# Optimization experiments

Hardware: AMD Instinct MI355X
Metric: run time of the kernel (lower is better)

## Reference

```python
import jax, jax.numpy as jnp
import numpy as np

N = 50000      # nodes
E = 800000     # edges (before self-loops)
F_IN = 128     # input node features
H = 4          # attention heads
C = 32         # hidden channels per head (concat width = H*C = 128)
CLS = 40       # num classes (layer 4, concat=False -> mean over heads)
NEG_SLOPE = 0.2


def setup_inputs() -> dict:
    key = jax.random.key(0)
    ks = jax.random.split(key, 16)
    w = lambda k, shape: (jax.random.normal(k, shape, jnp.float32) * 0.1)
    return {
        "x": jax.random.normal(ks[0], (N, F_IN), jnp.float32),
        "edge_index": jax.random.randint(ks[1], (2, E), 0, N),
        "W1": w(ks[2], (F_IN, H * C)), "att_src1": w(ks[3], (H, C)), "att_dst1": w(ks[4], (H, C)), "b1": jnp.zeros((H * C,), jnp.float32),
        "W2": w(ks[5], (H * C, H * C)), "att_src2": w(ks[6], (H, C)), "att_dst2": w(ks[7], (H, C)), "b2": jnp.zeros((H * C,), jnp.float32),
        "W3": w(ks[8], (H * C, H * C)), "att_src3": w(ks[9], (H, C)), "att_dst3": w(ks[10], (H, C)), "b3": jnp.zeros((H * C,), jnp.float32),
        "W4": w(ks[11], (H * C, H * CLS)), "att_src4": w(ks[12], (H, CLS)), "att_dst4": w(ks[13], (H, CLS)), "b4": jnp.zeros((CLS,), jnp.float32),
    }


def _gat(x, W, a_src, a_dst, b, src, dst, n, heads, ch, concat):
    # Linear transform, per-head view: [n, heads, ch]
    h = (x @ W).reshape(n, heads, ch)
    # per-node scalar attention terms [n, heads]
    es = (h * a_src).sum(-1)
    ed = (h * a_dst).sum(-1)
    # edge logits: alpha_j (source) + alpha_i (target), leaky relu (PyG GATConv)
    e = jax.nn.leaky_relu(es[src] + ed[dst], NEG_SLOPE)  # [Etot, heads]
    # segment softmax over incoming edges of each dst node (self-loops guarantee >=1 edge)
    m = jax.ops.segment_max(e, dst, num_segments=n)
    ealpha = jnp.exp(e - m[dst])
    denom = jax.ops.segment_sum(ealpha, dst, num_segments=n)
    alpha = ealpha / denom[dst]
    # weighted message aggregation (scatter-add)
    out = jax.ops.segment_sum(h[src] * alpha[:, :, None], dst, num_segments=n)
    out = out.reshape(n, heads * ch) if concat else out.mean(axis=1)
    return out + b


def reference(x, edge_index, W1, att_src1, att_dst1, b1, W2, att_src2, att_dst2, b2,
              W3, att_src3, att_dst3, b3, W4, att_src4, att_dst4, b4):
    n = x.shape[0]
    loop = jnp.arange(n)
    src = jnp.concatenate([edge_index[0], loop])  # add self-loops (PyG default)
    dst = jnp.concatenate([edge_index[1], loop])
    # dropout layers are identity in eval mode (training=False)
    h = _gat(x, W1, att_src1, att_dst1, b1, src, dst, n, H, C, True)
    h = jax.nn.relu(h)
    h = _gat(h, W2, att_src2, att_dst2, b2, src, dst, n, H, C, True)
    h = jax.nn.relu(h)
    h = _gat(h, W3, att_src3, att_dst3, b3, src, dst, n, H, C, True)
    h = jax.nn.relu(h)
    h = _gat(h, W4, att_src4, att_dst4, b4, src, dst, n, H, CLS, False)
    return h
```

## Files before the change

### kernel.cpp

```cpp
#include <hip/hip_runtime.h>
#include <math.h>

#define NN 50000
#define EE 800000
#define ET (EE + NN)
#define NCHK ((NN + 255) / 256)
#define NEG 0.2f

__device__ __forceinline__ float lrelu(float x) { return x > 0.f ? x : NEG * x; }

typedef __bf16 bf16x8 __attribute__((ext_vector_type(8)));
typedef float f32x4 __attribute__((ext_vector_type(4)));


__global__ __launch_bounds__(256) void k_hist(const int* __restrict__ eidx, int* __restrict__ cnt) {
    int i = blockIdx.x * 256 + threadIdx.x;
    if (i < EE) atomicAdd(&cnt[eidx[EE + i]], 1);
}

__global__ __launch_bounds__(256) void k_csum(const int* __restrict__ cnt, int* __restrict__ csums) {
    __shared__ int sh[256];
    int t = threadIdx.x, i = blockIdx.x * 256 + t;
    sh[t] = (i < NN) ? cnt[i] + 1 : 0;
    __syncthreads();
    for (int off = 128; off > 0; off >>= 1) {
        if (t < off) sh[t] += sh[t + off];
        __syncthreads();
    }
    if (t == 0) csums[blockIdx.x] = sh[0];
}

__global__ __launch_bounds__(256) void k_cscan(int* __restrict__ csums, int* __restrict__ rowptr) {
    __shared__ int sh[256];
    int t = threadIdx.x;
    sh[t] = (t < NCHK) ? csums[t] : 0;
    __syncthreads();
    for (int off = 1; off < 256; off <<= 1) {
        int x = (t >= off) ? sh[t - off] : 0;
        __syncthreads();
        sh[t] += x;
        __syncthreads();
    }
    int ex = (t == 0) ? 0 : sh[t - 1];
    if (t < NCHK) csums[t] = ex;
    if (t == 0) rowptr[NN] = ET;
}

__global__ __launch_bounds__(256) void k_chscan(const int* __restrict__ cnt, const int* __restrict__ csums,
                                                int* __restrict__ rowptr, int* __restrict__ cursor) {
    __shared__ int sh[256];
    int t = threadIdx.x, b = blockIdx.x, i = b * 256 + t;
    int v = (i < NN) ? cnt[i] + 1 : 0;
    sh[t] = v;
    __syncthreads();
    for (int off = 1; off < 256; off <<= 1) {
        int x = (t >= off) ? sh[t - off] : 0;
        __syncthreads();
        sh[t] += x;
        __syncthreads();
    }
    int ex = (t == 0 ? 0 : sh[t - 1]) + csums[b];
    if (i < NN) { rowptr[i] = ex; cursor[i] = ex; }
}

__global__ __launch_bounds__(256) void k_scatter(const int* __restrict__ eidx,
                                                 int* __restrict__ cursor, int* __restrict__ ssrc) {
    int i = blockIdx.x * 256 + threadIdx.x;
    if (i >= ET) return;
    int s, d;
    if (i < EE) { s = eidx[i]; d = eidx[EE + i]; } else { s = d = i - EE; }
    int pos = atomicAdd(&cursor[d], 1);
    ssrc[pos] = s;
}


template <int NOUT>
__global__ __launch_bounds__(256) void k_wsplit(const float* __restrict__ Wm,
                                                __bf16* __restrict__ Whi, __bf16* __restrict__ Wlo) {
    int i = blockIdx.x * 256 + threadIdx.x;
    if (i >= 128 * NOUT) return;
    int k = i / NOUT, c = i - k * NOUT;
    float v = Wm[i];
    __bf16 hi = (__bf16)v;
    __bf16 lo = (__bf16)(v - (float)hi);
    size_t off = ((size_t)(k >> 3) * NOUT + c) * 8 + (k & 7);
    Whi[off] = hi;
    Wlo[off] = lo;
}


template <int NOUT, bool FUSE>
__global__ __launch_bounds__(256) void k_gemm2(const float* __restrict__ X,
                                               const __bf16* __restrict__ Whi,
                                               const __bf16* __restrict__ Wlo,
                                               float* __restrict__ Y,
                                               const float* __restrict__ asrc,
                                               const float* __restrict__ adst,
                                               float* __restrict__ es, float* __restrict__ ed) {
    constexpr int NT = NOUT / 16;
    int tid = threadIdx.x;
    int w = tid >> 6, l = tid & 63;
    int col = l & 15, kg = l >> 4;
    int rb = blockIdx.x * 64;
    int arow = rb + w * 16 + col;
    int rclamp = arow < NN ? arow : NN - 1;
    f32x4 acc[NT];
    #pragma unroll
    for (int t = 0; t < NT; ++t) acc[t] = (f32x4){0.f, 0.f, 0.f, 0.f};

    #pragma unroll
    for (int c4 = 0; c4 < 4; ++c4) {
        float4 aA = *reinterpret_cast<const float4*>(&X[(size_t)rclamp * 128 + c4 * 32 + kg * 8]);
        float4 aB = *reinterpret_cast<const float4*>(&X[(size_t)rclamp * 128 + c4 * 32 + kg * 8 + 4]);
        float av[8] = {aA.x, aA.y, aA.z, aA.w, aB.x, aB.y, aB.z, aB.w};
        bf16x8 ahi, alo;
        #pragma unroll
        for (int j = 0; j < 8; ++j) {
            __bf16 h = (__bf16)av[j];
            ahi[j] = h;
            alo[j] = (__bf16)(av[j] - (float)h);
        }
        const __bf16* bh = Whi + ((size_t)(c4 * 4 + kg) * NOUT) * 8;
        const __bf16* bl = Wlo + ((size_t)(c4 * 4 + kg) * NOUT) * 8;
        #pragma unroll
        for (int t = 0; t < NT; ++t) {
            bf16x8 bhi = *reinterpret_cast<const bf16x8*>(bh + (t * 16 + col) * 8);
            bf16x8 blo = *reinterpret_cast<const bf16x8*>(bl + (t * 16 + col) * 8);
            acc[t] = __builtin_amdgcn_mfma_f32_16x16x32_bf16(ahi, bhi, acc[t], 0, 0, 0);
            acc[t] = __builtin_amdgcn_mfma_f32_16x16x32_bf16(alo, bhi, acc[t], 0, 0, 0);
            acc[t] = __builtin_amdgcn_mfma_f32_16x16x32_bf16(ahi, blo, acc[t], 0, 0, 0);
        }
    }

    #pragma unroll
    for (int t = 0; t < NT; ++t) {
        int cc = t * 16 + col;
        #pragma unroll
        for (int i = 0; i < 4; ++i) {
            int rr = rb + w * 16 + kg * 4 + i;
            if (rr < NN) Y[(size_t)rr * NOUT + cc] = acc[t][i];
        }
    }

    if constexpr (FUSE) {
        float pes[4][4], ped[4][4];
        #pragma unroll
        for (int h = 0; h < 4; ++h)
            #pragma unroll
            for (int i = 0; i < 4; ++i) { pes[h][i] = 0.f; ped[h][i] = 0.f; }
        #pragma unroll
        for (int t = 0; t < 8; ++t) {
            float as = asrc[t * 16 + col];
            float ad = adst[t * 16 + col];
            int h = t >> 1;
            #pragma unroll
            for (int i = 0; i < 4; ++i) {
                pes[h][i] += acc[t][i] * as;
                ped[h][i] += acc[t][i] * ad;
            }
        }
        #pragma unroll
        for (int off = 1; off < 16; off <<= 1) {
            #pragma unroll
            for (int h = 0; h < 4; ++h)
                #pragma unroll
                for (int i = 0; i < 4; ++i) {
                    pes[h][i] += __shfl_xor(pes[h][i], off);
                    ped[h][i] += __shfl_xor(ped[h][i], off);
                }
        }
        if (col == 0) {
            #pragma unroll
            for (int i = 0; i < 4; ++i) {
                int rr = rb + w * 16 + kg * 4 + i;
                if (rr < NN) {
                    #pragma unroll
                    for (int h = 0; h < 4; ++h) {
                        es[rr * 4 + h] = pes[h][i];
                        ed[rr * 4 + h] = ped[h][i];
                    }
                }
            }
        }
    }
}


template <int CH>
__global__ __launch_bounds__(256) void k_attn_scal(const float* __restrict__ Hf,
                                                   const float* __restrict__ asrc,
                                                   const float* __restrict__ adst,
                                                   float* __restrict__ es, float* __restrict__ ed) {
    int i = blockIdx.x * 256 + threadIdx.x;
    if (i >= NN * 4) return;
    int h = i & 3, n = i >> 2;
    const float4* row = reinterpret_cast<const float4*>(Hf + (size_t)n * (4 * CH) + h * CH);
    const float4* As  = reinterpret_cast<const float4*>(asrc + h * CH);
    const float4* Ad  = reinterpret_cast<const float4*>(adst + h * CH);
    float s = 0.f, d = 0.f;
    #pragma unroll
    for (int c = 0; c < CH / 4; ++c) {
        float4 v = row[c], a = As[c], b = Ad[c];
        s += v.x * a.x + v.y * a.y + v.z * a.z + v.w * a.w;
        d += v.x * b.x + v.y * b.y + v.z * b.z + v.w * b.w;
    }
    es[i] = s;
    ed[i] = d;
}


__global__ __launch_bounds__(256) void k_agg128(const float* __restrict__ Hf,
                                                const float* __restrict__ es, const float* __restrict__ ed,
                                                const int* __restrict__ rowptr, const int* __restrict__ ssrc,
                                                const float* __restrict__ bias, float* __restrict__ Yout) {
    int wid = (blockIdx.x * 256 + threadIdx.x) >> 6;
    int lane = threadIdx.x & 63;
    if (wid >= NN) return;
    int n = wid;
    int beg = rowptr[n], end = rowptr[n + 1];
    int h1 = lane & 3;
    int eoff = lane >> 2;
    float edv = ed[n * 4 + h1];

    float m = -1e30f, dsum = 0.f;
    for (int idx = beg + eoff; idx < end; idx += 16) {
        int s = ssrc[idx];
        float e = lrelu(es[s * 4 + h1] + edv);
        float M = fmaxf(m, e);
        dsum = dsum * __expf(m - M) + __expf(e - M);
        m = M;
    }
    #pragma unroll
    for (int off = 4; off < 64; off <<= 1) {
        float om = __shfl_xor(m, off);
        float od = __shfl_xor(dsum, off);
        float M = fmaxf(m, om);
        dsum = dsum * __expf(m - M) + od * __expf(om - M);
        m = M;
    }
    float invd = 1.f / dsum;

    int q = lane & 7;
    int eg8 = lane >> 3;
    f32x4 acc4[4];
    #pragma unroll
    for (int i = 0; i < 4; ++i) acc4[i] = (f32x4){0.f, 0.f, 0.f, 0.f};

    int nch = (end - beg + 15) >> 4;
    int base = beg;
    for (int ch = 0; ch < nch; ++ch, base += 16) {
        int myIdx = base + eoff;
        int s = ssrc[myIdx < end ? myIdx : end - 1];
        float e = lrelu(es[s * 4 + h1] + edv);
        float alpha = (myIdx < end) ? __expf(e - m) * invd : 0.f;
        #pragma unroll
        for (int hb = 0; hb < 2; ++hb) {
            int e16 = hb * 8 + eg8;
            int se = __shfl(s, e16 * 4);
            const float* rowp = Hf + (size_t)se * 128 + q * 4;
            #pragma unroll
            for (int i = 0; i < 4; ++i) {
                float p = __shfl(alpha, e16 * 4 + i);
                float4 v = *reinterpret_cast<const float4*>(rowp + i * 32);
                acc4[i].x += p * v.x;
                acc4[i].y += p * v.y;
                acc4[i].z += p * v.z;
                acc4[i].w += p * v.w;
            }
        }
    }

    #pragma unroll
    for (int off = 8; off < 64; off <<= 1) {
        #pragma unroll
        for (int i = 0; i < 4; ++i) {
            acc4[i].x += __shfl_xor(acc4[i].x, off);
            acc4[i].y += __shfl_xor(acc4[i].y, off);
            acc4[i].z += __shfl_xor(acc4[i].z, off);
            acc4[i].w += __shfl_xor(acc4[i].w, off);
        }
    }
    if (lane < 8) {
        #pragma unroll
        for (int i = 0; i < 4; ++i) {
            int c0 = 32 * i + 4 * lane;
            float4 bv = *reinterpret_cast<const float4*>(&bias[c0]);
            float4 o;
            o.x = fmaxf(acc4[i].x + bv.x, 0.f);
            o.y = fmaxf(acc4[i].y + bv.y, 0.f);
            o.z = fmaxf(acc4[i].z + bv.z, 0.f);
            o.w = fmaxf(acc4[i].w + bv.w, 0.f);
            *reinterpret_cast<float4*>(&Yout[(size_t)n * 128 + c0]) = o;
        }
    }
}


__global__ __launch_bounds__(256) void k_agg160_mean(const float* __restrict__ Hf,
                                                     const float* __restrict__ es, const float* __restrict__ ed,
                                                     const int* __restrict__ rowptr, const int* __restrict__ ssrc,
                                                     const float* __restrict__ b4, float* __restrict__ out) {
    __shared__ float buf[4][160];
    int wid = (blockIdx.x * 256 + threadIdx.x) >> 6;
    int lane = threadIdx.x & 63;
    int w = threadIdx.x >> 6;
    if (wid >= NN) return;
    int n = wid;
    int beg = rowptr[n], end = rowptr[n + 1];
    int h1 = lane & 3;
    int eoff = lane >> 2;
    float edv = ed[n * 4 + h1];

    float m = -1e30f, dsum = 0.f;
    for (int idx = beg + eoff; idx < end; idx += 16) {
        int s = ssrc[idx];
        float e = lrelu(es[s * 4 + h1] + edv);
        float M = fmaxf(m, e);
        dsum = dsum * __expf(m - M) + __expf(e - M);
        m = M;
    }
    #pragma unroll
    for (int off = 4; off < 64; off <<= 1) {
        float om = __shfl_xor(m, off);
        float od = __shfl_xor(dsum, off);
        float M = fmaxf(m, om);
        dsum = dsum * __expf(m - M) + od * __expf(om - M);
        m = M;
    }
    float invd = 1.f / dsum;

    int q = lane & 7;
    int eg8 = lane >> 3;
    int hh[5];
    #pragma unroll
    for (int i = 0; i < 5; ++i) hh[i] = (i * 8 + q) / 10;
    f32x4 acc4[5];
    #pragma unroll
    for (int i = 0; i < 5; ++i) acc4[i] = (f32x4){0.f, 0.f, 0.f, 0.f};

    int nch = (end - beg + 15) >> 4;
    int base = beg;
    for (int ch = 0; ch < nch; ++ch, base += 16) {
        int myIdx = base + eoff;
        int s = ssrc[myIdx < end ? myIdx : end - 1];
        float e = lrelu(es[s * 4 + h1] + edv);
        float alpha = (myIdx < end) ? __expf(e - m) * invd : 0.f;
        #pragma unroll
        for (int hb = 0; hb < 2; ++hb) {
            int e16 = hb * 8 + eg8;
            int se = __shfl(s, e16 * 4);
            const float* rowp = Hf + (size_t)se * 160 + q * 4;
            #pragma unroll
            for (int i = 0; i < 5; ++i) {
                float p = __shfl(alpha, e16 * 4 + hh[i]);
                float4 v = *reinterpret_cast<const float4*>(rowp + i * 32);
                acc4[i].x += p * v.x;
                acc4[i].y += p * v.y;
                acc4[i].z += p * v.z;
                acc4[i].w += p * v.w;
            }
        }
    }

    #pragma unroll
    for (int off = 8; off < 64; off <<= 1) {
        #pragma unroll
        for (int i = 0; i < 5; ++i) {
            acc4[i].x += __shfl_xor(acc4[i].x, off);
            acc4[i].y += __shfl_xor(acc4[i].y, off);
            acc4[i].z += __shfl_xor(acc4[i].z, off);
            acc4[i].w += __shfl_xor(acc4[i].w, off);
        }
    }
    if (lane < 8) {
        #pragma unroll
        for (int i = 0; i < 5; ++i)
            *reinterpret_cast<float4*>(&buf[w][32 * i + 4 * lane]) = (float4){acc4[i].x, acc4[i].y, acc4[i].z, acc4[i].w};
    }
    __builtin_amdgcn_wave_barrier();
    if (lane < 40) {
        float v = 0.25f * (buf[w][lane] + buf[w][lane + 40] + buf[w][lane + 80] + buf[w][lane + 120]) + b4[lane];
        out[(size_t)n * 40 + lane] = v;
    }
}


extern "C" void kernel_launch(void* const* d_in, const int* in_sizes, int n_in,
                              void* d_out, int out_size, void* d_ws, size_t ws_size,
                              hipStream_t stream) {
    const float* x    = (const float*)d_in[0];
    const int*   eidx = (const int*)d_in[1];
    const float* W[4]    = {(const float*)d_in[2], (const float*)d_in[6], (const float*)d_in[10], (const float*)d_in[14]};
    const float* asrc[4] = {(const float*)d_in[3], (const float*)d_in[7], (const float*)d_in[11], (const float*)d_in[15]};
    const float* adst[4] = {(const float*)d_in[4], (const float*)d_in[8], (const float*)d_in[12], (const float*)d_in[16]};
    const float* bias[4] = {(const float*)d_in[5], (const float*)d_in[9], (const float*)d_in[13], (const float*)d_in[17]};
    float* out = (float*)d_out;

    float* hA = (float*)d_ws;
    float* hB = hA + (size_t)NN * 160;
    float* es = hB + (size_t)NN * 160;
    float* ed = es + (size_t)NN * 4;
    int* rowptr = (int*)(ed + (size_t)NN * 4);
    int* cnt    = rowptr + (NN + 1);
    int* cursor = cnt + NN;
    int* ssrc   = cursor + NN;
    int* csums  = ssrc + ET;
    __bf16* wsp = (__bf16*)(csums + 256);
    __bf16* Whi[4], *Wlo[4];
    {
        __bf16* p = wsp;
        for (int i = 0; i < 4; ++i) {
            int sz = 128 * (i == 3 ? 160 : 128);
            Whi[i] = p; p += sz;
            Wlo[i] = p; p += sz;
        }
    }

    hipMemsetAsync(cnt, 0, NN * sizeof(int), stream);
    k_hist<<<(EE + 255) / 256, 256, 0, stream>>>(eidx, cnt);
    k_csum<<<NCHK, 256, 0, stream>>>(cnt, csums);
    k_cscan<<<1, 256, 0, stream>>>(csums, rowptr);
    k_chscan<<<NCHK, 256, 0, stream>>>(cnt, csums, rowptr, cursor);
    k_scatter<<<(ET + 255) / 256, 256, 0, stream>>>(eidx, cursor, ssrc);

    k_wsplit<128><<<(128 * 128 + 255) / 256, 256, 0, stream>>>(W[0], Whi[0], Wlo[0]);
    k_wsplit<128><<<(128 * 128 + 255) / 256, 256, 0, stream>>>(W[1], Whi[1], Wlo[1]);
    k_wsplit<128><<<(128 * 128 + 255) / 256, 256, 0, stream>>>(W[2], Whi[2], Wlo[2]);
    k_wsplit<160><<<(128 * 160 + 255) / 256, 256, 0, stream>>>(W[3], Whi[3], Wlo[3]);

    int gemmBlocks = (NN + 63) / 64;
    int aggBlocks = (NN * 64 + 255) / 256;

    k_gemm2<128, true><<<gemmBlocks, 256, 0, stream>>>(x, Whi[0], Wlo[0], hA, asrc[0], adst[0], es, ed);
    k_agg128<<<aggBlocks, 256, 0, stream>>>(hA, es, ed, rowptr, ssrc, bias[0], hB);

    k_gemm2<128, true><<<gemmBlocks, 256, 0, stream>>>(hB, Whi[1], Wlo[1], hA, asrc[1], adst[1], es, ed);
    k_agg128<<<aggBlocks, 256, 0, stream>>>(hA, es, ed, rowptr, ssrc, bias[1], hB);

    k_gemm2<128, true><<<gemmBlocks, 256, 0, stream>>>(hB, Whi[2], Wlo[2], hA, asrc[2], adst[2], es, ed);
    k_agg128<<<aggBlocks, 256, 0, stream>>>(hA, es, ed, rowptr, ssrc, bias[2], hB);

    k_gemm2<160, false><<<gemmBlocks, 256, 0, stream>>>(hB, Whi[3], Wlo[3], hA, nullptr, nullptr, nullptr, nullptr);
    k_attn_scal<40><<<(NN * 4 + 255) / 256, 256, 0, stream>>>(hA, asrc[3], adst[3], es, ed);
    k_agg160_mean<<<aggBlocks, 256, 0, stream>>>(hA, es, ed, rowptr, ssrc, bias[3], out);
}
```

Measured before the change: 500.9 us.

## Merge scan and weight-split launches, widen GEMM tiles, fuse layer-4 attention scalars

Result: faster. 473.8 us (-5.4%).

```diff
diff --git a/kernel.cpp b/kernel.cpp
--- a/kernel.cpp
+++ b/kernel.cpp
@@ -30,37 +30,27 @@
     if (t == 0) csums[blockIdx.x] = sh[0];
 }
 
-__global__ __launch_bounds__(256) void k_cscan(int* __restrict__ csums, int* __restrict__ rowptr) {
-    __shared__ int sh[256];
-    int t = threadIdx.x;
-    sh[t] = (t < NCHK) ? csums[t] : 0;
-    __syncthreads();
-    for (int off = 1; off < 256; off <<= 1) {
-        int x = (t >= off) ? sh[t - off] : 0;
-        __syncthreads();
-        sh[t] += x;
-        __syncthreads();
-    }
-    int ex = (t == 0) ? 0 : sh[t - 1];
-    if (t < NCHK) csums[t] = ex;
-    if (t == 0) rowptr[NN] = ET;
-}
-
 __global__ __launch_bounds__(256) void k_chscan(const int* __restrict__ cnt, const int* __restrict__ csums,
                                                 int* __restrict__ rowptr, int* __restrict__ cursor) {
     __shared__ int sh[256];
+    __shared__ int shc[256];
     int t = threadIdx.x, b = blockIdx.x, i = b * 256 + t;
     int v = (i < NN) ? cnt[i] + 1 : 0;
     sh[t] = v;
+    shc[t] = (t < NCHK) ? csums[t] : 0;
     __syncthreads();
     for (int off = 1; off < 256; off <<= 1) {
-        int x = (t >= off) ? sh[t - off] : 0;
+        int x1 = (t >= off) ? sh[t - off] : 0;
+        int x2 = (t >= off) ? shc[t - off] : 0;
         __syncthreads();
-        sh[t] += x;
+        sh[t] += x1;
+        shc[t] += x2;
         __syncthreads();
     }
-    int ex = (t == 0 ? 0 : sh[t - 1]) + csums[b];
+    int cbase = (b == 0) ? 0 : shc[b - 1];
+    int ex = (t == 0 ? 0 : sh[t - 1]) + cbase;
     if (i < NN) { rowptr[i] = ex; cursor[i] = ex; }
+    if (b == 0 && t == 0) rowptr[NN] = ET;
 }
 
 __global__ __launch_bounds__(256) void k_scatter(const int* __restrict__ eidx,
@@ -74,23 +64,28 @@
 }
 
 
-template <int NOUT>
-__global__ __launch_bounds__(256) void k_wsplit(const float* __restrict__ Wm,
-                                                __bf16* __restrict__ Whi, __bf16* __restrict__ Wlo) {
+__global__ __launch_bounds__(256) void k_wsplit_all(const float* __restrict__ W0, const float* __restrict__ W1,
+                                                    const float* __restrict__ W2, const float* __restrict__ W3,
+                                                    __bf16* __restrict__ wsp) {
     int i = blockIdx.x * 256 + threadIdx.x;
-    if (i >= 128 * NOUT) return;
-    int k = i / NOUT, c = i - k * NOUT;
-    float v = Wm[i];
+    const float* Wm; int NOUT, j; size_t base, sz;
+    if (i < 16384)      { Wm = W0; NOUT = 128; j = i;          base = 0;     sz = 16384; }
+    else if (i < 32768) { Wm = W1; NOUT = 128; j = i - 16384;  base = 32768; sz = 16384; }
+    else if (i < 49152) { Wm = W2; NOUT = 128; j = i - 32768;  base = 65536; sz = 16384; }
+    else if (i < 69632) { Wm = W3; NOUT = 160; j = i - 49152;  base = 98304; sz = 20480; }
+    else return;
+    float v = Wm[j];
+    int k = j / NOUT, c = j - k * NOUT;
     __bf16 hi = (__bf16)v;
     __bf16 lo = (__bf16)(v - (float)hi);
-    size_t off = ((size_t)(k >> 3) * NOUT + c) * 8 + (k & 7);
-    Whi[off] = hi;
-    Wlo[off] = lo;
+    size_t off = base + ((size_t)(k >> 3) * NOUT + c) * 8 + (k & 7);
+    wsp[off] = hi;
+    wsp[off + sz] = lo;
 }
 
 
 template <int NOUT, bool FUSE>
-__global__ __launch_bounds__(256) void k_gemm2(const float* __restrict__ X,
+__global__ __launch_bounds__(256) void k_gemm3(const float* __restrict__ X,
                                                const __bf16* __restrict__ Whi,
                                                const __bf16* __restrict__ Wlo,
                                                float* __restrict__ Y,
@@ -98,27 +93,35 @@
                                                const float* __restrict__ adst,
                                                float* __restrict__ es, float* __restrict__ ed) {
     constexpr int NT = NOUT / 16;
+    constexpr int CH = NOUT / 4;
     int tid = threadIdx.x;
     int w = tid >> 6, l = tid & 63;
     int col = l & 15, kg = l >> 4;
-    int rb = blockIdx.x * 64;
-    int arow = rb + w * 16 + col;
-    int rclamp = arow < NN ? arow : NN - 1;
-    f32x4 acc[NT];
-    #pragma unroll
-    for (int t = 0; t < NT; ++t) acc[t] = (f32x4){0.f, 0.f, 0.f, 0.f};
+    int rb = blockIdx.x * 128 + w * 32;
+    int r0 = rb + col, r1 = rb + 16 + col;
+    int rc0 = r0 < NN ? r0 : NN - 1;
+    int rc1 = r1 < NN ? r1 : NN - 1;
+
+    f32x4 acc0[NT], acc1[NT];
+    #pragma unroll
+    for (int t = 0; t < NT; ++t) { acc0[t] = (f32x4){0,0,0,0}; acc1[t] = (f32x4){0,0,0,0}; }
 
     #pragma unroll
     for (int c4 = 0; c4 < 4; ++c4) {
-        float4 aA = *reinterpret_cast<const float4*>(&X[(size_t)rclamp * 128 + c4 * 32 + kg * 8]);
-        float4 aB = *reinterpret_cast<const float4*>(&X[(size_t)rclamp * 128 + c4 * 32 + kg * 8 + 4]);
-        float av[8] = {aA.x, aA.y, aA.z, aA.w, aB.x, aB.y, aB.z, aB.w};
-        bf16x8 ahi, alo;
-        #pragma unroll
-        for (int j = 0; j < 8; ++j) {
-            __bf16 h = (__bf16)av[j];
-            ahi[j] = h;
-            alo[j] = (__bf16)(av[j] - (float)h);
+        bf16x8 ah0, al0, ah1, al1;
+        {
+            float4 aA = *reinterpret_cast<const float4*>(&X[(size_t)rc0 * 128 + c4 * 32 + kg * 8]);
+            float4 aB = *reinterpret_cast<const float4*>(&X[(size_t)rc0 * 128 + c4 * 32 + kg * 8 + 4]);
+            float av[8] = {aA.x, aA.y, aA.z, aA.w, aB.x, aB.y, aB.z, aB.w};
+            #pragma unroll
+            for (int j = 0; j < 8; ++j) { __bf16 h = (__bf16)av[j]; ah0[j] = h; al0[j] = (__bf16)(av[j] - (float)h); }
+        }
+        {
+            float4 aA = *reinterpret_cast<const float4*>(&X[(size_t)rc1 * 128 + c4 * 32 + kg * 8]);
+            float4 aB = *reinterpret_cast<const float4*>(&X[(size_t)rc1 * 128 + c4 * 32 + kg * 8 + 4]);
+            float av[8] = {aA.x, aA.y, aA.z, aA.w, aB.x, aB.y, aB.z, aB.w};
+            #pragma unroll
+            for (int j = 0; j < 8; ++j) { __bf16 h = (__bf16)av[j]; ah1[j] = h; al1[j] = (__bf16)(av[j] - (float)h); }
         }
         const __bf16* bh = Whi + ((size_t)(c4 * 4 + kg) * NOUT) * 8;
         const __bf16* bl = Wlo + ((size_t)(c4 * 4 + kg) * NOUT) * 8;
@@ -126,9 +129,12 @@
         for (int t = 0; t < NT; ++t) {
             bf16x8 bhi = *reinterpret_cast<const bf16x8*>(bh + (t * 16 + col) * 8);
             bf16x8 blo = *reinterpret_cast<const bf16x8*>(bl + (t * 16 + col) * 8);
-            acc[t] = __builtin_amdgcn_mfma_f32_16x16x32_bf16(ahi, bhi, acc[t], 0, 0, 0);
-            acc[t] = __builtin_amdgcn_mfma_f32_16x16x32_bf16(alo, bhi, acc[t], 0, 0, 0);
-            acc[t] = __builtin_amdgcn_mfma_f32_16x16x32_bf16(ahi, blo, acc[t], 0, 0, 0);
+            acc0[t] = __builtin_amdgcn_mfma_f32_16x16x32_bf16(ah0, bhi, acc0[t], 0, 0, 0);
+            acc0[t] = __builtin_amdgcn_mfma_f32_16x16x32_bf16(al0, bhi, acc0[t], 0, 0, 0);
+            acc0[t] = __builtin_amdgcn_mfma_f32_16x16x32_bf16(ah0, blo, acc0[t], 0, 0, 0);
+            acc1[t] = __builtin_amdgcn_mfma_f32_16x16x32_bf16(ah1, bhi, acc1[t], 0, 0, 0);
+            acc1[t] = __builtin_amdgcn_mfma_f32_16x16x32_bf16(al1, bhi, acc1[t], 0, 0, 0);
+            acc1[t] = __builtin_amdgcn_mfma_f32_16x16x32_bf16(ah1, blo, acc1[t], 0, 0, 0);
         }
     }
 
@@ -137,75 +143,74 @@
         int cc = t * 16 + col;
         #pragma unroll
         for (int i = 0; i < 4; ++i) {
-            int rr = rb + w * 16 + kg * 4 + i;
-            if (rr < NN) Y[(size_t)rr * NOUT + cc] = acc[t][i];
+            int ra = rb + kg * 4 + i;
+            int rbq = rb + 16 + kg * 4 + i;
+            if (ra < NN)  Y[(size_t)ra  * NOUT + cc] = acc0[t][i];
+            if (rbq < NN) Y[(size_t)rbq * NOUT + cc] = acc1[t][i];
         }
     }
 
     if constexpr (FUSE) {
-        float pes[4][4], ped[4][4];
-        #pragma unroll
-        for (int h = 0; h < 4; ++h)
-            #pragma unroll
-            for (int i = 0; i < 4; ++i) { pes[h][i] = 0.f; ped[h][i] = 0.f; }
-        #pragma unroll
-        for (int t = 0; t < 8; ++t) {
+        float pes[2][4][4], ped[2][4][4];
+        #pragma unroll
+        for (int rt = 0; rt < 2; ++rt)
+            #pragma unroll
+            for (int h = 0; h < 4; ++h)
+                #pragma unroll
+                for (int i = 0; i < 4; ++i) { pes[rt][h][i] = 0.f; ped[rt][h][i] = 0.f; }
+        #pragma unroll
+        for (int t = 0; t < NT; ++t) {
             float as = asrc[t * 16 + col];
             float ad = adst[t * 16 + col];
-            int h = t >> 1;
-            #pragma unroll
-            for (int i = 0; i < 4; ++i) {
-                pes[h][i] += acc[t][i] * as;
-                ped[h][i] += acc[t][i] * ad;
-            }
-        }
-        #pragma unroll
-        for (int off = 1; off < 16; off <<= 1) {
-            #pragma unroll
-            for (int h = 0; h < 4; ++h)
+            int hA = (t * 16) / CH;
+            int hB = (t * 16 + 15) / CH;
+            if (hA == hB) {
                 #pragma unroll
                 for (int i = 0; i < 4; ++i) {
-                    pes[h][i] += __shfl_xor(pes[h][i], off);
-                    ped[h][i] += __shfl_xor(ped[h][i], off);
+                    pes[0][hA][i] += acc0[t][i] * as;  ped[0][hA][i] += acc0[t][i] * ad;
+                    pes[1][hA][i] += acc1[t][i] * as;  ped[1][hA][i] += acc1[t][i] * ad;
                 }
+            } else {
+                bool isB = (col >= (hB * CH - t * 16));
+                #pragma unroll
+                for (int i = 0; i < 4; ++i) {
+                    float vs0 = acc0[t][i] * as, vd0 = acc0[t][i] * ad;
+                    float vs1 = acc1[t][i] * as, vd1 = acc1[t][i] * ad;
+                    pes[0][hA][i] += isB ? 0.f : vs0;  pes[0][hB][i] += isB ? vs0 : 0.f;
+                    ped[0][hA][i] += isB ? 0.f : vd0;  ped[0][hB][i] += isB ? vd0 : 0.f;
+                    pes[1][hA][i] += isB ? 0.f : vs1;  pes[1][hB][i] += isB ? vs1 : 0.f;
+                    ped[1][hA][i] += isB ? 0.f : vd1;  ped[1][hB][i] += isB ? vd1 : 0.f;
+                }
+            }
+        }
+        #pragma unroll
+        for (int off = 1; off < 16; off <<= 1) {
+            #pragma unroll
+            for (int rt = 0; rt < 2; ++rt)
+                #pragma unroll
+                for (int h = 0; h < 4; ++h)
+                    #pragma unroll
+                    for (int i = 0; i < 4; ++i) {
+                        pes[rt][h][i] += __shfl_xor(pes[rt][h][i], off);
+                        ped[rt][h][i] += __shfl_xor(ped[rt][h][i], off);
+                    }
         }
         if (col == 0) {
             #pragma unroll
-            for (int i = 0; i < 4; ++i) {
-                int rr = rb + w * 16 + kg * 4 + i;
-                if (rr < NN) {
-                    #pragma unroll
-                    for (int h = 0; h < 4; ++h) {
-                        es[rr * 4 + h] = pes[h][i];
-                        ed[rr * 4 + h] = ped[h][i];
+            for (int rt = 0; rt < 2; ++rt)
+                #pragma unroll
+                for (int i = 0; i < 4; ++i) {
+                    int rr = rb + rt * 16 + kg * 4 + i;
+                    if (rr < NN) {
+                        #pragma unroll
+                        for (int h = 0; h < 4; ++h) {
+                            es[rr * 4 + h] = pes[rt][h][i];
+                            ed[rr * 4 + h] = ped[rt][h][i];
+                        }
                     }
                 }
-            }
-        }
-    }
-}
-
-
-template <int CH>
-__global__ __launch_bounds__(256) void k_attn_scal(const float* __restrict__ Hf,
-                                                   const float* __restrict__ asrc,
-                                                   const float* __restrict__ adst,
-                                                   float* __restrict__ es, float* __restrict__ ed) {
-    int i = blockIdx.x * 256 + threadIdx.x;
-    if (i >= NN * 4) return;
-    int h = i & 3, n = i >> 2;
-    const float4* row = reinterpret_cast<const float4*>(Hf + (size_t)n * (4 * CH) + h * CH);
-    const float4* As  = reinterpret_cast<const float4*>(asrc + h * CH);
-    const float4* Ad  = reinterpret_cast<const float4*>(adst + h * CH);
-    float s = 0.f, d = 0.f;
-    #pragma unroll
-    for (int c = 0; c < CH / 4; ++c) {
-        float4 v = row[c], a = As[c], b = Ad[c];
-        s += v.x * a.x + v.y * a.y + v.z * a.z + v.w * a.w;
-        d += v.x * b.x + v.y * b.y + v.z * b.z + v.w * b.w;
-    }
-    es[i] = s;
-    ed[i] = d;
+        }
+    }
 }
 
 
@@ -419,28 +424,23 @@
     hipMemsetAsync(cnt, 0, NN * sizeof(int), stream);
     k_hist<<<(EE + 255) / 256, 256, 0, stream>>>(eidx, cnt);
     k_csum<<<NCHK, 256, 0, stream>>>(cnt, csums);
-    k_cscan<<<1, 256, 0, stream>>>(csums, rowptr);
     k_chscan<<<NCHK, 256, 0, stream>>>(cnt, csums, rowptr, cursor);
     k_scatter<<<(ET + 255) / 256, 256, 0, stream>>>(eidx, cursor, ssrc);
 
-    k_wsplit<128><<<(128 * 128 + 255) / 256, 256, 0, stream>>>(W[0], Whi[0], Wlo[0]);
-    k_wsplit<128><<<(128 * 128 + 255) / 256, 256, 0, stream>>>(W[1], Whi[1], Wlo[1]);
-    k_wsplit<128><<<(128 * 128 + 255) / 256, 256, 0, stream>>>(W[2], Whi[2], Wlo[2]);
-    k_wsplit<160><<<(128 * 160 + 255) / 256, 256, 0, stream>>>(W[3], Whi[3], Wlo[3]);
-
-    int gemmBlocks = (NN + 63) / 64;
+    k_wsplit_all<<<(69632 + 255) / 256, 256, 0, stream>>>(W[0], W[1], W[2], W[3], wsp);
+
+    int gemmBlocks = (NN + 127) / 128;
     int aggBlocks = (NN * 64 + 255) / 256;
 
-    k_gemm2<128, true><<<gemmBlocks, 256, 0, stream>>>(x, Whi[0], Wlo[0], hA, asrc[0], adst[0], es, ed);
+    k_gemm3<128, true><<<gemmBlocks, 256, 0, stream>>>(x, Whi[0], Wlo[0], hA, asrc[0], adst[0], es, ed);
     k_agg128<<<aggBlocks, 256, 0, stream>>>(hA, es, ed, rowptr, ssrc, bias[0], hB);
 
-    k_gemm2<128, true><<<gemmBlocks, 256, 0, stream>>>(hB, Whi[1], Wlo[1], hA, asrc[1], adst[1], es, ed);
+    k_gemm3<128, true><<<gemmBlocks, 256, 0, stream>>>(hB, Whi[1], Wlo[1], hA, asrc[1], adst[1], es, ed);
     k_agg128<<<aggBlocks, 256, 0, stream>>>(hA, es, ed, rowptr, ssrc, bias[1], hB);
 
-    k_gemm2<128, true><<<gemmBlocks, 256, 0, stream>>>(hB, Whi[2], Wlo[2], hA, asrc[2], adst[2], es, ed);
+    k_gemm3<128, true><<<gemmBlocks, 256, 0, stream>>>(hB, Whi[2], Wlo[2], hA, asrc[2], adst[2], es, ed);
     k_agg128<<<aggBlocks, 256, 0, stream>>>(hA, es, ed, rowptr, ssrc, bias[2], hB);
 
-    k_gemm2<160, false><<<gemmBlocks, 256, 0, stream>>>(hB, Whi[3], Wlo[3], hA, nullptr, nullptr, nullptr, nullptr);
-    k_attn_scal<40><<<(NN * 4 + 255) / 256, 256, 0, stream>>>(hA, asrc[3], adst[3], es, ed);
+    k_gemm3<160, true><<<gemmBlocks, 256, 0, stream>>>(hB, Whi[3], Wlo[3], hA, asrc[3], adst[3], es, ed);
     k_agg160_mean<<<aggBlocks, 256, 0, stream>>>(hA, es, ed, rowptr, ssrc, bias[3], out);
 }
```
